# Kernel optimization log

Measured on AMD Instinct MI355X. Metric: run time of the kernel, lower is better.

The kernel has to match this reference:

```python
import jax, jax.numpy as jnp
import numpy as np

N, T, K, V, E = 64, 256, 64, 32000, 100


def setup_inputs() -> dict:
    key = jax.random.key(0)
    ks = jax.random.split(key, 7)
    x = jax.random.randint(ks[0], (N, T), 0, V)
    emb_weight = jax.random.normal(ks[1], (V, E), dtype=jnp.float32)
    # trans: Linear(E, K*K, bias=False), weight uniform(-1,1)
    W_trans = jax.random.uniform(ks[2], (K * K, E), minval=-1.0, maxval=1.0, dtype=jnp.float32)
    # start: Linear(1, K)
    start_w = jax.random.normal(ks[3], (K, 1), dtype=jnp.float32) * 0.1
    start_b = jax.random.normal(ks[4], (K,), dtype=jnp.float32) * 0.1
    # emb_cluster: Embedding(K, K)
    emb_cluster_w = jax.random.normal(ks[5], (K, K), dtype=jnp.float32)
    # vocab: Linear(K, V, bias=False), weight uniform(-1,1)
    vocab_w = jax.random.uniform(ks[6], (V, K), minval=-1.0, maxval=1.0, dtype=jnp.float32)
    return {"x": x, "emb_weight": emb_weight, "W_trans": W_trans,
            "start_w": start_w, "start_b": start_b,
            "emb_cluster_w": emb_cluster_w, "vocab_w": vocab_w}


def reference(x, emb_weight, W_trans, start_w, start_b, emb_cluster_w, vocab_w):
    n, t = x.shape
    k = emb_cluster_w.shape[0]
    # word embeddings used to condition transitions at steps 0..T-2
    xe = emb_weight[x[:, :-1]]                                   # [N,T-1,E]
    # transition log-probs: log_softmax over destination state
    tran = jax.nn.log_softmax(
        jnp.einsum('nte,ce->ntc', xe, W_trans).reshape(n, t - 1, k, k), axis=-1)
    # emission log-probs per cluster: E[k, v]
    Elog = jax.nn.log_softmax(emb_cluster_w @ vocab_w.T, axis=-1)  # [K,V]
    emit = Elog.T[x[:, 1:]]                                       # [N,T-1,K]
    # initial alpha: log_softmax(start(ones)) expanded over batch
    alpha0 = jax.nn.log_softmax(start_w[:, 0] + start_b)           # [K]
    alpha0 = jnp.broadcast_to(alpha0[None, :], (n, k))
    tran_t = jnp.moveaxis(tran, 1, 0)   # [T-1,N,K,K]
    emit_t = jnp.moveaxis(emit, 1, 0)   # [T-1,N,K]

    def step(alpha, te):
        tr, em = te
        # logsumexp over previous state j: alpha[n,j] + tr[n,j,k]
        a = jax.scipy.special.logsumexp(alpha[:, :, None] + tr, axis=1) + em
        return a, None

    alpha, _ = jax.lax.scan(step, alpha0, (tran_t, emit_t))
    return -jnp.mean(jax.scipy.special.logsumexp(alpha, axis=1))
```

## Files before the change

kernel.cpp:

```cpp
#include <hip/hip_runtime.h>
#include <hip/hip_bf16.h>
#include <stdint.h>

#define NT 16320
#define NTPAD 16384
#define KDIM 128
#define NCOLS 4096
#define NSEQ 64
#define TSTEPS 255
#define VOCAB 32000
#define EDIM 100
#define CHUNKS 17
#define CLEN 15

typedef __attribute__((ext_vector_type(8))) short s8v;
typedef __attribute__((ext_vector_type(4))) float f4v;

__device__ __forceinline__ float bflo(uint32_t u) { return __uint_as_float(u << 16); }
__device__ __forceinline__ float bfhi(uint32_t u) { return __uint_as_float(u & 0xffff0000u); }

__device__ __forceinline__ void load_lds16(const void* g, void* l) {
    __builtin_amdgcn_global_load_lds(
        (const __attribute__((address_space(1))) void*)(uintptr_t)g,
        (__attribute__((address_space(3))) void*)(uintptr_t)l,
        16, 0, 0);
}

__global__ __launch_bounds__(256) void prep_dk(const int* __restrict__ x,
                                               const float* __restrict__ emb,
                                               const float* __restrict__ Wt,
                                               const float* __restrict__ ec,
                                               const float* __restrict__ vw,
                                               __hip_bfloat16* __restrict__ A,
                                               __hip_bfloat16* __restrict__ B,
                                               float* __restrict__ partials) {
    int bid = blockIdx.x;
    int tid = threadIdx.x;
    if (bid < 1280) {
        int rloc = tid >> 4, q = tid & 15;
        int b = bid * 16 + rloc;
        int c0 = q * 8;
        float vals[8] = {0.f, 0.f, 0.f, 0.f, 0.f, 0.f, 0.f, 0.f};
        __hip_bfloat16* dst;
        if (b < NTPAD) {
            if (b < NT) {
                int n = b / TSTEPS;
                int t = b - n * TSTEPS;
                int tok = x[n * 256 + t];
                const float* er = emb + (size_t)tok * EDIM;
#pragma unroll
                for (int i = 0; i < 8; ++i) { int e = c0 + i; if (e < EDIM) vals[i] = er[e]; }
            }
            dst = A + (size_t)b * KDIM + c0;
        } else {
            int cc = b - NTPAD;
            const float* wr = Wt + (size_t)cc * EDIM;
#pragma unroll
            for (int i = 0; i < 8; ++i) { int e = c0 + i; if (e < EDIM) vals[i] = wr[e]; }
            dst = B + (size_t)cc * KDIM + c0;
        }
        union { __hip_bfloat16 h[8]; uint4 u; } pk;
#pragma unroll
        for (int i = 0; i < 8; ++i) pk.h[i] = __float2bfloat16(vals[i]);
        *(uint4*)dst = pk.u;
    } else {
        int db = bid - 1280;
        int wave = tid >> 6, lane = tid & 63;
        float er[64];
        {
            const float4* ecv = (const float4*)(ec + (size_t)lane * 64);
#pragma unroll
            for (int i = 0; i < 16; ++i) {
                float4 v = ecv[i];
                er[4 * i] = v.x; er[4 * i + 1] = v.y; er[4 * i + 2] = v.z; er[4 * i + 3] = v.w;
            }
        }
        int v0 = db * 125;
        float m = -1e30f, s = 0.f;
        for (int v = v0 + wave; v < v0 + 125; v += 4) {
            int vu = __builtin_amdgcn_readfirstlane(v);
            const float* row = vw + (size_t)vu * 64;
            float acc = 0.f;
#pragma unroll
            for (int e = 0; e < 64; ++e) acc += er[e] * row[e];
            float nm = fmaxf(m, acc);
            s = s * __expf(m - nm) + __expf(acc - nm);
            m = nm;
        }
        __shared__ float pm[4][64], ps[4][64];
        pm[wave][lane] = m; ps[wave][lane] = s;
        __syncthreads();
        if (tid < 64) {
            float M = pm[0][tid], Ssum = ps[0][tid];
#pragma unroll
            for (int w = 1; w < 4; ++w) {
                float m2 = pm[w][tid], s2 = ps[w][tid];
                float nm = fmaxf(M, m2);
                Ssum = Ssum * __expf(M - nm) + s2 * __expf(m2 - nm);
                M = nm;
            }
            partials[(db * 64 + tid) * 2]     = M;
            partials[(db * 64 + tid) * 2 + 1] = Ssum;
        }
    }
}

__global__ __launch_bounds__(256) void emit_kern(const int* __restrict__ x,
                                                 const float* __restrict__ ec,
                                                 const float* __restrict__ vw,
                                                 const float* __restrict__ partials,
                                                 __hip_bfloat16* __restrict__ emB) {
    __shared__ float pm[4][64], ps[4][64], sD[64];
    int tid = threadIdx.x;
    int wave = tid >> 6, lane = tid & 63;

    {
        float M = -1e30f, S = 0.f;
        for (int b = wave; b < 256; b += 4) {
            float m2 = partials[(b * 64 + lane) * 2];
            float s2 = partials[(b * 64 + lane) * 2 + 1];
            float nm = fmaxf(M, m2);
            S = S * __expf(M - nm) + s2 * __expf(m2 - nm);
            M = nm;
        }
        pm[wave][lane] = M; ps[wave][lane] = S;
    }

    float er[64];
    {
        const float4* ecv = (const float4*)(ec + (size_t)lane * 64);
#pragma unroll
        for (int i = 0; i < 16; ++i) {
            float4 v = ecv[i];
            er[4 * i] = v.x; er[4 * i + 1] = v.y; er[4 * i + 2] = v.z; er[4 * i + 3] = v.w;
        }
    }
    __syncthreads();
    if (tid < 64) {
        float M = pm[0][tid], S = ps[0][tid];
#pragma unroll
        for (int w = 1; w < 4; ++w) {
            float m2 = pm[w][tid], s2 = ps[w][tid];
            float nm = fmaxf(M, m2);
            S = S * __expf(M - nm) + s2 * __expf(m2 - nm);
            M = nm;
        }
        sD[tid] = M + __logf(S);
    }
    __syncthreads();

    float dj = sD[lane];
    int j = lane;
    int pos = ((j >> 2) & 3) * 16 + ((j >> 4) & 3) * 4 + (j & 3);
    int nt0 = blockIdx.x * 32 + wave * 8;
#pragma unroll
    for (int s = 0; s < 8; ++s) {
        int nt = nt0 + s;
        int n = nt / TSTEPS;
        int t = nt - n * TSTEPS;
        int tok = x[n * 256 + t + 1];
        tok = __builtin_amdgcn_readfirstlane(tok);
        const float* row = vw + (size_t)tok * 64;
        float acc = 0.f;
#pragma unroll
        for (int e = 0; e < 64; ++e) acc += er[e] * row[e];
        emB[(size_t)nt * 64 + pos] = __float2bfloat16(__expf(acc - dj));
    }
}

__global__ __launch_bounds__(256) void gemm_kern(const __hip_bfloat16* __restrict__ A,
                                                 const __hip_bfloat16* __restrict__ B,
                                                 const __hip_bfloat16* __restrict__ emB,
                                                 __hip_bfloat16* __restrict__ Eg) {
    int mblk = blockIdx.x;
    int nblk = blockIdx.y;
    int tid = threadIdx.x, wave = tid >> 6, lane = tid & 63;

    __shared__ __align__(16) char smem[65536];
    char* sA = smem;
    char* sB = smem + 32768;

    {
        int r0 = wave * 32;
        int l16 = lane & 15;
        int rsub = lane >> 4;
#pragma unroll
        for (int g = 0; g < 8; ++g) {
            int r = r0 + g * 4 + rsub;
            int chunk = l16 ^ (r & 7);
            const char* gp = (const char*)(A + (size_t)(mblk * 128 + r) * KDIM) + chunk * 16;
            load_lds16(gp, sA + (r0 + g * 4) * 256);
        }
#pragma unroll
        for (int g = 0; g < 8; ++g) {
            int c = r0 + g * 4 + rsub;
            int chunk = l16 ^ (c & 7);
            const char* gp = (const char*)(B + (size_t)(nblk * 128 + c) * KDIM) + chunk * 16;
            load_lds16(gp, sB + (r0 + g * 4) * 256);
        }
    }
    __syncthreads();

    int wc = (wave >> 1) * 64, wm = (wave & 1) * 64;
    int l15 = lane & 15, g4 = lane >> 4;
    f4v acc[4][4] = {};
#pragma unroll
    for (int k32 = 0; k32 < 4; ++k32) {
        s8v af[4], bf[4];
#pragma unroll
        for (int jt = 0; jt < 4; ++jt) {
            int r = wc + jt * 16 + l15;
            int chunk = (k32 * 4 + g4) ^ (r & 7);
            af[jt] = *(const s8v*)(sB + r * 256 + chunk * 16);
        }
#pragma unroll
        for (int mt = 0; mt < 4; ++mt) {
            int r = wm + mt * 16 + l15;
            int chunk = (k32 * 4 + g4) ^ (r & 7);
            bf[mt] = *(const s8v*)(sA + r * 256 + chunk * 16);
        }
#pragma unroll
        for (int jt = 0; jt < 4; ++jt)
#pragma unroll
            for (int mt = 0; mt < 4; ++mt)
                acc[jt][mt] = __builtin_amdgcn_mfma_f32_16x16x32_bf16(af[jt], bf[mt], acc[jt][mt], 0, 0, 0);
    }
    __syncthreads();

    char* sW = smem;
    const char* emb8 = (const char*)emB;
#pragma unroll
    for (int mt = 0; mt < 4; ++mt) {
        int mrow = wm + mt * 16 + l15;
        int mglob = mblk * 128 + mrow;
        float v[16];
#pragma unroll
        for (int jt = 0; jt < 4; ++jt)
#pragma unroll
            for (int rr = 0; rr < 4; ++rr) v[jt * 4 + rr] = acc[jt][mt][rr];
        float mx = v[0];
#pragma unroll
        for (int k = 1; k < 16; ++k) mx = fmaxf(mx, v[k]);
        mx = fmaxf(mx, __shfl_xor(mx, 16, 64));
        mx = fmaxf(mx, __shfl_xor(mx, 32, 64));
        float ex[16], sg = 0.f;
#pragma unroll
        for (int k = 0; k < 16; ++k) { ex[k] = __expf(v[k] - mx); sg += ex[k]; }
        sg += __shfl_xor(sg, 16, 64);
        sg += __shfl_xor(sg, 32, 64);
        float inv = 1.0f / sg;
        uint4 e0 = *(const uint4*)(emb8 + (size_t)mglob * 128 + g4 * 32);
        uint4 e1 = *(const uint4*)(emb8 + (size_t)mglob * 128 + g4 * 32 + 16);
        float em[16];
        {
            const uint32_t* w0 = (const uint32_t*)&e0;
            const uint32_t* w1 = (const uint32_t*)&e1;
#pragma unroll
            for (int i = 0; i < 4; ++i) {
                em[2 * i] = bflo(w0[i]);     em[2 * i + 1] = bfhi(w0[i]);
                em[8 + 2 * i] = bflo(w1[i]); em[8 + 2 * i + 1] = bfhi(w1[i]);
            }
        }
#pragma unroll
        for (int jt = 0; jt < 4; ++jt) {
            union { __hip_bfloat16 h[4]; uint2 u; } pk;
#pragma unroll
            for (int rr = 0; rr < 4; ++rr)
                pk.h[rr] = __float2bfloat16(ex[jt * 4 + rr] * inv * em[jt * 4 + rr]);
            *(uint2*)(sW + mrow * 272 + (wc + jt * 16 + g4 * 4) * 2) = pk.u;
        }
    }
    __syncthreads();

    {
        int rloc = tid >> 3;
        int q = tid & 7;
#pragma unroll
        for (int rp = 0; rp < 4; ++rp) {
            int row = rp * 32 + rloc;
            char* dst = (char*)Eg + (size_t)(mblk * 128 + row) * 8192 + nblk * 256;
            const char* src = sW + row * 272;
            *(uint4*)(dst + q * 16)       = *(const uint4*)(src + q * 16);
            *(uint4*)(dst + 128 + q * 16) = *(const uint4*)(src + 128 + q * 16);
        }
    }
}

__global__ __launch_bounds__(64) void chunk_kern(const __hip_bfloat16* __restrict__ Eg,
                                                 __hip_bfloat16* __restrict__ Gout,
                                                 float* __restrict__ Rout,
                                                 float* __restrict__ out) {
    int lane = threadIdx.x;
    if (blockIdx.x == 0 && lane == 0) *out = 0.f;
    int l15 = lane & 15, g4 = lane >> 4;
    int id = blockIdx.x;
    int n = (id * 3856) >> 16;
    int c = id - n * 17;
    int base_m = n * TSTEPS + c * CLEN;

    __shared__ __align__(16) char sGT[64 * 144];

    {
        uint4 z = {0, 0, 0, 0};
#pragma unroll
        for (int i = 0; i < 8; ++i) *(uint4*)(sGT + lane * 144 + i * 16) = z;
        *(uint16_t*)(sGT + lane * 144 + lane * 2) = 0x3F80;
    }

    const char* Ebase = (const char*)Eg;
    uint4 pf[4][2];
    {
        const char* tp = Ebase + (size_t)(base_m + 14) * 8192;
#pragma unroll
        for (int at = 0; at < 4; ++at)
#pragma unroll
            for (int kk = 0; kk < 2; ++kk)
                pf[at][kk] = *(const uint4*)(tp + (at * 16 + l15) * 128 + kk * 64 + g4 * 16);
    }

    float rlog[4] = {0.f, 0.f, 0.f, 0.f};

    for (int tl = 14; tl >= 0; --tl) {
        uint4 af[4][2];
#pragma unroll
        for (int at = 0; at < 4; ++at) { af[at][0] = pf[at][0]; af[at][1] = pf[at][1]; }
        if (tl > 0) {
            const char* tp = Ebase + (size_t)(base_m + tl - 1) * 8192;
#pragma unroll
            for (int at = 0; at < 4; ++at)
#pragma unroll
                for (int kk = 0; kk < 2; ++kk)
                    pf[at][kk] = *(const uint4*)(tp + (at * 16 + l15) * 128 + kk * 64 + g4 * 16);
        }

        f4v acc[4][4] = {};
#pragma unroll
        for (int kk = 0; kk < 2; ++kk) {
#pragma unroll
            for (int ct = 0; ct < 4; ++ct) {
                s8v b = *(const s8v*)(sGT + (ct * 16 + l15) * 144 + kk * 64 + g4 * 16);
#pragma unroll
                for (int at = 0; at < 4; ++at)
                    acc[at][ct] = __builtin_amdgcn_mfma_f32_16x16x32_bf16(
                        *(const s8v*)&af[at][kk], b, acc[at][ct], 0, 0, 0);
            }
        }

        if (tl % 3 == 0) {
#pragma unroll
            for (int ct = 0; ct < 4; ++ct) {
                float mx = acc[0][ct][0];
#pragma unroll
                for (int at = 0; at < 4; ++at)
#pragma unroll
                    for (int rr = 0; rr < 4; ++rr) mx = fmaxf(mx, acc[at][ct][rr]);
                mx = fmaxf(mx, __shfl_xor(mx, 16, 64));
                mx = fmaxf(mx, __shfl_xor(mx, 32, 64));
                mx = fmaxf(mx, 1e-38f);
                rlog[ct] += __logf(mx);
                float inv = 1.0f / mx;
                int col = ct * 16 + l15;
#pragma unroll
                for (int at = 0; at < 4; ++at) {
                    union { __hip_bfloat16 h[4]; uint2 u; } pk;
#pragma unroll
                    for (int rr = 0; rr < 4; ++rr)
                        pk.h[rr] = __float2bfloat16(acc[at][ct][rr] * inv);
                    *(uint2*)(sGT + col * 144 + at * 32 + g4 * 8) = pk.u;
                }
            }
        } else {
#pragma unroll
            for (int ct = 0; ct < 4; ++ct) {
                int col = ct * 16 + l15;
#pragma unroll
                for (int at = 0; at < 4; ++at) {
                    union { __hip_bfloat16 h[4]; uint2 u; } pk;
#pragma unroll
                    for (int rr = 0; rr < 4; ++rr)
                        pk.h[rr] = __float2bfloat16(acc[at][ct][rr]);
                    *(uint2*)(sGT + col * 144 + at * 32 + g4 * 8) = pk.u;
                }
            }
        }
    }

    {
        char* go = (char*)(Gout + (size_t)id * 4096 + lane * 64);
#pragma unroll
        for (int i = 0; i < 8; ++i)
            *(uint4*)(go + i * 16) = *(const uint4*)(sGT + lane * 144 + i * 16);
    }
    if (g4 == 0)
#pragma unroll
        for (int ct = 0; ct < 4; ++ct)
            Rout[(size_t)id * 64 + ct * 16 + l15] = rlog[ct];
}

__global__ __launch_bounds__(64) void combine_kern(const __hip_bfloat16* __restrict__ G,
                                                   const float* __restrict__ R,
                                                   const float* __restrict__ sw,
                                                   const float* __restrict__ sb,
                                                   float* __restrict__ out) {
    int n = blockIdx.x;
    int lane = threadIdx.x;
    __shared__ __align__(16) float sV[64];

    float alpha;
    {
        float v = sw[lane] + sb[lane];
        float m = v;
#pragma unroll
        for (int off = 1; off < 64; off <<= 1) m = fmaxf(m, __shfl_xor(m, off, 64));
        float s = __expf(v - m);
#pragma unroll
        for (int off = 1; off < 64; off <<= 1) s += __shfl_xor(s, off, 64);
        alpha = v - (m + __logf(s));
    }

    const char* Gb = (const char*)(G + (size_t)n * CHUNKS * 4096) + lane * 128;
    const float* Rb = R + (size_t)n * CHUNKS * 64 + lane;

    uint4 pf[8];
#pragma unroll
    for (int i = 0; i < 8; ++i) pf[i] = *(const uint4*)(Gb + i * 16);
    float rpf = Rb[0];

    for (int c = 0; c < CHUNKS; ++c) {
        uint4 cur[8];
#pragma unroll
        for (int i = 0; i < 8; ++i) cur[i] = pf[i];
        float rc = rpf;
        if (c + 1 < CHUNKS) {
            const char* gn = Gb + (size_t)(c + 1) * 8192;
#pragma unroll
            for (int i = 0; i < 8; ++i) pf[i] = *(const uint4*)(gn + i * 16);
            rpf = Rb[(c + 1) * 64];
        }

        float m = alpha;
#pragma unroll
        for (int off = 1; off < 64; off <<= 1) m = fmaxf(m, __shfl_xor(m, off, 64));
        sV[lane] = __expf(alpha - m);
        float acc = 0.f;
        const float4* sv4 = (const float4*)sV;
#pragma unroll
        for (int i = 0; i < 8; ++i) {
            const uint32_t* gw = (const uint32_t*)&cur[i];
            float4 va = sv4[2 * i], vb = sv4[2 * i + 1];
            acc += va.x * bflo(gw[0]) + va.y * bfhi(gw[0]);
            acc += va.z * bflo(gw[1]) + va.w * bfhi(gw[1]);
            acc += vb.x * bflo(gw[2]) + vb.y * bfhi(gw[2]);
            acc += vb.z * bflo(gw[3]) + vb.w * bfhi(gw[3]);
        }
        alpha = m + __logf(fmaxf(acc, 1e-38f)) + rc;
    }

    {
        float m = alpha;
#pragma unroll
        for (int off = 1; off < 64; off <<= 1) m = fmaxf(m, __shfl_xor(m, off, 64));
        float s = __expf(alpha - m);
#pragma unroll
        for (int off = 1; off < 64; off <<= 1) s += __shfl_xor(s, off, 64);
        if (lane == 0) atomicAdd(out, -(m + __logf(s)) * (1.0f / 64.0f));
    }
}

extern "C" void kernel_launch(void* const* d_in, const int* in_sizes, int n_in,
                              void* d_out, int out_size, void* d_ws, size_t ws_size,
                              hipStream_t stream) {
    const int*   x   = (const int*)d_in[0];
    const float* emb = (const float*)d_in[1];
    const float* Wt  = (const float*)d_in[2];
    const float* sw  = (const float*)d_in[3];
    const float* sb  = (const float*)d_in[4];
    const float* ec  = (const float*)d_in[5];
    const float* vw  = (const float*)d_in[6];
    float* out = (float*)d_out;
    char* ws = (char*)d_ws;

    __hip_bfloat16* Eg  = (__hip_bfloat16*)ws;
    __hip_bfloat16* A   = (__hip_bfloat16*)(ws + 134217728ull);
    __hip_bfloat16* B   = (__hip_bfloat16*)(ws + 138412032ull);
    __hip_bfloat16* emB = (__hip_bfloat16*)(ws + 139460608ull);
    float* partials     = (float*)(ws + 141557760ull);
    __hip_bfloat16* Gc  = (__hip_bfloat16*)(ws + 141688832ull);
    float* Rc           = (float*)(ws + 150601728ull);

    prep_dk<<<1536, 256, 0, stream>>>(x, emb, Wt, ec, vw, A, B, partials);
    emit_kern<<<510, 256, 0, stream>>>(x, ec, vw, partials, emB);
    gemm_kern<<<dim3(NTPAD / 128, NCOLS / 128), 256, 0, stream>>>(A, B, emB, Eg);
    chunk_kern<<<NSEQ * CHUNKS, 64, 0, stream>>>(Eg, Gc, Rc, out);
    combine_kern<<<NSEQ, 64, 0, stream>>>(Gc, Rc, sw, sb, out);
}
```

Measured before the change: 212.6 us.

## Fuse transition GEMM into chunked scan kernel, keep transition matrices in LDS

Merges the transition-matrix GEMM and the chunked scan into one kernel. Each block computes the 15 timestep transition matrices for its chunk straight into a swizzled LDS buffer, so the 128MB Eg intermediate no longer round-trips through global memory. The scan now runs across 4 waves, one column tile each, using about 129KB of dynamic LDS. In exchange, each block re-reads all of B from global/L2, and occupancy drops to one block per CU.

```diff
diff --git a/kernel.cpp b/kernel.cpp
--- a/kernel.cpp
+++ b/kernel.cpp
@@ -5,7 +5,6 @@
 #define NT 16320
 #define NTPAD 16384
 #define KDIM 128
-#define NCOLS 4096
 #define NSEQ 64
 #define TSTEPS 255
 #define VOCAB 32000
@@ -18,13 +17,6 @@
 
 __device__ __forceinline__ float bflo(uint32_t u) { return __uint_as_float(u << 16); }
 __device__ __forceinline__ float bfhi(uint32_t u) { return __uint_as_float(u & 0xffff0000u); }
-
-__device__ __forceinline__ void load_lds16(const void* g, void* l) {
-    __builtin_amdgcn_global_load_lds(
-        (const __attribute__((address_space(1))) void*)(uintptr_t)g,
-        (__attribute__((address_space(3))) void*)(uintptr_t)l,
-        16, 0, 0);
-}
 
 __global__ __launch_bounds__(256) void prep_dk(const int* __restrict__ x,
                                                const float* __restrict__ emb,
@@ -168,76 +160,74 @@
     }
 }
 
-__global__ __launch_bounds__(256) void gemm_kern(const __hip_bfloat16* __restrict__ A,
-                                                 const __hip_bfloat16* __restrict__ B,
-                                                 const __hip_bfloat16* __restrict__ emB,
-                                                 __hip_bfloat16* __restrict__ Eg) {
-    int mblk = blockIdx.x;
-    int nblk = blockIdx.y;
-    int tid = threadIdx.x, wave = tid >> 6, lane = tid & 63;
-
-    __shared__ __align__(16) char smem[65536];
-    char* sA = smem;
-    char* sB = smem + 32768;
-
-    {
-        int r0 = wave * 32;
-        int l16 = lane & 15;
-        int rsub = lane >> 4;
-#pragma unroll
-        for (int g = 0; g < 8; ++g) {
-            int r = r0 + g * 4 + rsub;
-            int chunk = l16 ^ (r & 7);
-            const char* gp = (const char*)(A + (size_t)(mblk * 128 + r) * KDIM) + chunk * 16;
-            load_lds16(gp, sA + (r0 + g * 4) * 256);
-        }
-#pragma unroll
-        for (int g = 0; g < 8; ++g) {
-            int c = r0 + g * 4 + rsub;
-            int chunk = l16 ^ (c & 7);
-            const char* gp = (const char*)(B + (size_t)(nblk * 128 + c) * KDIM) + chunk * 16;
-            load_lds16(gp, sB + (r0 + g * 4) * 256);
-        }
-    }
-    __syncthreads();
-
-    int wc = (wave >> 1) * 64, wm = (wave & 1) * 64;
+__global__ __launch_bounds__(256, 1) void fused_kern(const __hip_bfloat16* __restrict__ A,
+                                                     const __hip_bfloat16* __restrict__ B,
+                                                     const __hip_bfloat16* __restrict__ emB,
+                                                     __hip_bfloat16* __restrict__ Gout,
+                                                     float* __restrict__ Rout,
+                                                     float* __restrict__ out) {
+    extern __shared__ __align__(16) char smem[];
+    char* sE  = smem;
+    char* sGT = smem + 122880;
+
+    int tid = threadIdx.x;
+    int wave = tid >> 6, lane = tid & 63;
     int l15 = lane & 15, g4 = lane >> 4;
-    f4v acc[4][4] = {};
-#pragma unroll
-    for (int k32 = 0; k32 < 4; ++k32) {
-        s8v af[4], bf[4];
-#pragma unroll
-        for (int jt = 0; jt < 4; ++jt) {
-            int r = wc + jt * 16 + l15;
-            int chunk = (k32 * 4 + g4) ^ (r & 7);
-            af[jt] = *(const s8v*)(sB + r * 256 + chunk * 16);
-        }
-#pragma unroll
-        for (int mt = 0; mt < 4; ++mt) {
-            int r = wm + mt * 16 + l15;
-            int chunk = (k32 * 4 + g4) ^ (r & 7);
-            bf[mt] = *(const s8v*)(sA + r * 256 + chunk * 16);
-        }
+    int id = blockIdx.x;
+    if (id == 0 && tid == 0) *out = 0.f;
+    int n = (id * 3856) >> 16;
+    int c = id - n * 17;
+    int base_m = n * TSTEPS + c * CLEN;
+
+    if (wave == 0) {
+        uint4 z = {0, 0, 0, 0};
+#pragma unroll
+        for (int i = 0; i < 8; ++i) *(uint4*)(sGT + lane * 144 + i * 16) = z;
+        *(uint16_t*)(sGT + lane * 144 + lane * 2) = 0x3F80;
+    }
+
+    const char* Ac = (const char*)A;
+    s8v bfx[4];
+#pragma unroll
+    for (int k32 = 0; k32 < 4; ++k32)
+        bfx[k32] = *(const s8v*)(Ac + (size_t)(base_m + l15) * 256 + k32 * 64 + g4 * 16);
+
+    float em[16];
+    {
+        const char* ep = (const char*)emB + (size_t)(base_m + l15) * 128 + g4 * 32;
+        uint4 e0 = *(const uint4*)ep;
+        uint4 e1 = *(const uint4*)(ep + 16);
+        const uint32_t* w0 = (const uint32_t*)&e0;
+        const uint32_t* w1 = (const uint32_t*)&e1;
+#pragma unroll
+        for (int i = 0; i < 4; ++i) {
+            em[2 * i] = bflo(w0[i]);     em[2 * i + 1] = bfhi(w0[i]);
+            em[8 + 2 * i] = bflo(w1[i]); em[8 + 2 * i + 1] = bfhi(w1[i]);
+        }
+    }
+
+    const char* Bc = (const char*)B;
+    for (int grp = 0; grp < 16; ++grp) {
+        int gidx = wave * 16 + grp;
+        int cbase = gidx * 64;
+        s8v af[4][4];
 #pragma unroll
         for (int jt = 0; jt < 4; ++jt)
 #pragma unroll
-            for (int mt = 0; mt < 4; ++mt)
-                acc[jt][mt] = __builtin_amdgcn_mfma_f32_16x16x32_bf16(af[jt], bf[mt], acc[jt][mt], 0, 0, 0);
-    }
-    __syncthreads();
-
-    char* sW = smem;
-    const char* emb8 = (const char*)emB;
-#pragma unroll
-    for (int mt = 0; mt < 4; ++mt) {
-        int mrow = wm + mt * 16 + l15;
-        int mglob = mblk * 128 + mrow;
+            for (int k32 = 0; k32 < 4; ++k32)
+                af[jt][k32] = *(const s8v*)(Bc + (size_t)(cbase + jt * 16 + l15) * 256 + k32 * 64 + g4 * 16);
+        f4v acc[4] = {};
+#pragma unroll
+        for (int k32 = 0; k32 < 4; ++k32)
+#pragma unroll
+            for (int jt = 0; jt < 4; ++jt)
+                acc[jt] = __builtin_amdgcn_mfma_f32_16x16x32_bf16(af[jt][k32], bfx[k32], acc[jt], 0, 0, 0);
+
         float v[16];
 #pragma unroll
         for (int jt = 0; jt < 4; ++jt)
 #pragma unroll
-            for (int rr = 0; rr < 4; ++rr) v[jt * 4 + rr] = acc[jt][mt][rr];
+            for (int rr = 0; rr < 4; ++rr) v[jt * 4 + rr] = acc[jt][rr];
         float mx = v[0];
 #pragma unroll
         for (int k = 1; k < 16; ++k) mx = fmaxf(mx, v[k]);
@@ -249,152 +239,83 @@
         sg += __shfl_xor(sg, 16, 64);
         sg += __shfl_xor(sg, 32, 64);
         float inv = 1.0f / sg;
-        uint4 e0 = *(const uint4*)(emb8 + (size_t)mglob * 128 + g4 * 32);
-        uint4 e1 = *(const uint4*)(emb8 + (size_t)mglob * 128 + g4 * 32 + 16);
-        float em[16];
-        {
-            const uint32_t* w0 = (const uint32_t*)&e0;
-            const uint32_t* w1 = (const uint32_t*)&e1;
-#pragma unroll
-            for (int i = 0; i < 4; ++i) {
-                em[2 * i] = bflo(w0[i]);     em[2 * i + 1] = bfhi(w0[i]);
-                em[8 + 2 * i] = bflo(w1[i]); em[8 + 2 * i + 1] = bfhi(w1[i]);
-            }
-        }
-#pragma unroll
-        for (int jt = 0; jt < 4; ++jt) {
-            union { __hip_bfloat16 h[4]; uint2 u; } pk;
-#pragma unroll
-            for (int rr = 0; rr < 4; ++rr)
-                pk.h[rr] = __float2bfloat16(ex[jt * 4 + rr] * inv * em[jt * 4 + rr]);
-            *(uint2*)(sW + mrow * 272 + (wc + jt * 16 + g4 * 4) * 2) = pk.u;
+        if (l15 < 15) {
+            int swz = ((l15 ^ gidx) & 7) << 4;
+#pragma unroll
+            for (int jt = 0; jt < 4; ++jt) {
+                union { __hip_bfloat16 h[4]; uint2 u; } pk;
+#pragma unroll
+                for (int rr = 0; rr < 4; ++rr)
+                    pk.h[rr] = __float2bfloat16(ex[jt * 4 + rr] * inv * em[jt * 4 + rr]);
+                int off = l15 * 8192 + (cbase + jt * 16 + g4 * 4) * 2;
+                *(uint2*)(sE + (off ^ swz)) = pk.u;
+            }
         }
     }
     __syncthreads();
 
-    {
-        int rloc = tid >> 3;
-        int q = tid & 7;
-#pragma unroll
-        for (int rp = 0; rp < 4; ++rp) {
-            int row = rp * 32 + rloc;
-            char* dst = (char*)Eg + (size_t)(mblk * 128 + row) * 8192 + nblk * 256;
-            const char* src = sW + row * 272;
-            *(uint4*)(dst + q * 16)       = *(const uint4*)(src + q * 16);
-            *(uint4*)(dst + 128 + q * 16) = *(const uint4*)(src + 128 + q * 16);
-        }
-    }
-}
-
-__global__ __launch_bounds__(64) void chunk_kern(const __hip_bfloat16* __restrict__ Eg,
-                                                 __hip_bfloat16* __restrict__ Gout,
-                                                 float* __restrict__ Rout,
-                                                 float* __restrict__ out) {
-    int lane = threadIdx.x;
-    if (blockIdx.x == 0 && lane == 0) *out = 0.f;
-    int l15 = lane & 15, g4 = lane >> 4;
-    int id = blockIdx.x;
-    int n = (id * 3856) >> 16;
-    int c = id - n * 17;
-    int base_m = n * TSTEPS + c * CLEN;
-
-    __shared__ __align__(16) char sGT[64 * 144];
-
-    {
-        uint4 z = {0, 0, 0, 0};
-#pragma unroll
-        for (int i = 0; i < 8; ++i) *(uint4*)(sGT + lane * 144 + i * 16) = z;
-        *(uint16_t*)(sGT + lane * 144 + lane * 2) = 0x3F80;
-    }
-
-    const char* Ebase = (const char*)Eg;
-    uint4 pf[4][2];
-    {
-        const char* tp = Ebase + (size_t)(base_m + 14) * 8192;
+    int ct = wave;
+    int colrow = (ct * 16 + l15) * 144;
+    float rlog = 0.f;
+    for (int tl = 14; tl >= 0; --tl) {
+        int swz = ((tl ^ l15) & 7) << 4;
+        s8v af[4][2];
 #pragma unroll
         for (int at = 0; at < 4; ++at)
 #pragma unroll
-            for (int kk = 0; kk < 2; ++kk)
-                pf[at][kk] = *(const uint4*)(tp + (at * 16 + l15) * 128 + kk * 64 + g4 * 16);
-    }
-
-    float rlog[4] = {0.f, 0.f, 0.f, 0.f};
-
-    for (int tl = 14; tl >= 0; --tl) {
-        uint4 af[4][2];
-#pragma unroll
-        for (int at = 0; at < 4; ++at) { af[at][0] = pf[at][0]; af[at][1] = pf[at][1]; }
-        if (tl > 0) {
-            const char* tp = Ebase + (size_t)(base_m + tl - 1) * 8192;
+            for (int kk = 0; kk < 2; ++kk) {
+                int off = tl * 8192 + (at * 16 + l15) * 128 + kk * 64 + g4 * 16;
+                af[at][kk] = *(const s8v*)(sE + (off ^ swz));
+            }
+        s8v bG[2];
+#pragma unroll
+        for (int kk = 0; kk < 2; ++kk)
+            bG[kk] = *(const s8v*)(sGT + colrow + kk * 64 + g4 * 16);
+        f4v acc[4] = {};
+#pragma unroll
+        for (int kk = 0; kk < 2; ++kk)
 #pragma unroll
             for (int at = 0; at < 4; ++at)
-#pragma unroll
-                for (int kk = 0; kk < 2; ++kk)
-                    pf[at][kk] = *(const uint4*)(tp + (at * 16 + l15) * 128 + kk * 64 + g4 * 16);
-        }
-
-        f4v acc[4][4] = {};
-#pragma unroll
-        for (int kk = 0; kk < 2; ++kk) {
-#pragma unroll
-            for (int ct = 0; ct < 4; ++ct) {
-                s8v b = *(const s8v*)(sGT + (ct * 16 + l15) * 144 + kk * 64 + g4 * 16);
-#pragma unroll
-                for (int at = 0; at < 4; ++at)
-                    acc[at][ct] = __builtin_amdgcn_mfma_f32_16x16x32_bf16(
-                        *(const s8v*)&af[at][kk], b, acc[at][ct], 0, 0, 0);
-            }
-        }
+                acc[at] = __builtin_amdgcn_mfma_f32_16x16x32_bf16(af[at][kk], bG[kk], acc[at], 0, 0, 0);
 
         if (tl % 3 == 0) {
-#pragma unroll
-            for (int ct = 0; ct < 4; ++ct) {
-                float mx = acc[0][ct][0];
-#pragma unroll
-                for (int at = 0; at < 4; ++at)
-#pragma unroll
-                    for (int rr = 0; rr < 4; ++rr) mx = fmaxf(mx, acc[at][ct][rr]);
-                mx = fmaxf(mx, __shfl_xor(mx, 16, 64));
-                mx = fmaxf(mx, __shfl_xor(mx, 32, 64));
-                mx = fmaxf(mx, 1e-38f);
-                rlog[ct] += __logf(mx);
-                float inv = 1.0f / mx;
-                int col = ct * 16 + l15;
-#pragma unroll
-                for (int at = 0; at < 4; ++at) {
-                    union { __hip_bfloat16 h[4]; uint2 u; } pk;
-#pragma unroll
-                    for (int rr = 0; rr < 4; ++rr)
-                        pk.h[rr] = __float2bfloat16(acc[at][ct][rr] * inv);
-                    *(uint2*)(sGT + col * 144 + at * 32 + g4 * 8) = pk.u;
-                }
+            float mx = acc[0][0];
+#pragma unroll
+            for (int at = 0; at < 4; ++at)
+#pragma unroll
+                for (int rr = 0; rr < 4; ++rr) mx = fmaxf(mx, acc[at][rr]);
+            mx = fmaxf(mx, __shfl_xor(mx, 16, 64));
+            mx = fmaxf(mx, __shfl_xor(mx, 32, 64));
+            mx = fmaxf(mx, 1e-38f);
+            rlog += __logf(mx);
+            float inv = 1.0f / mx;
+#pragma unroll
+            for (int at = 0; at < 4; ++at) {
+                union { __hip_bfloat16 h[4]; uint2 u; } pk;
+#pragma unroll
+                for (int rr = 0; rr < 4; ++rr)
+                    pk.h[rr] = __float2bfloat16(acc[at][rr] * inv);
+                *(uint2*)(sGT + colrow + at * 32 + g4 * 8) = pk.u;
             }
         } else {
 #pragma unroll
-            for (int ct = 0; ct < 4; ++ct) {
-                int col = ct * 16 + l15;
-#pragma unroll
-                for (int at = 0; at < 4; ++at) {
-                    union { __hip_bfloat16 h[4]; uint2 u; } pk;
-#pragma unroll
-                    for (int rr = 0; rr < 4; ++rr)
-                        pk.h[rr] = __float2bfloat16(acc[at][ct][rr]);
-                    *(uint2*)(sGT + col * 144 + at * 32 + g4 * 8) = pk.u;
-                }
-            }
-        }
-    }
-
-    {
-        char* go = (char*)(Gout + (size_t)id * 4096 + lane * 64);
-#pragma unroll
-        for (int i = 0; i < 8; ++i)
-            *(uint4*)(go + i * 16) = *(const uint4*)(sGT + lane * 144 + i * 16);
-    }
-    if (g4 == 0)
-#pragma unroll
-        for (int ct = 0; ct < 4; ++ct)
-            Rout[(size_t)id * 64 + ct * 16 + l15] = rlog[ct];
+            for (int at = 0; at < 4; ++at) {
+                union { __hip_bfloat16 h[4]; uint2 u; } pk;
+#pragma unroll
+                for (int rr = 0; rr < 4; ++rr)
+                    pk.h[rr] = __float2bfloat16(acc[at][rr]);
+                *(uint2*)(sGT + colrow + at * 32 + g4 * 8) = pk.u;
+            }
+        }
+    }
+
+    {
+        char* go = (char*)(Gout + (size_t)id * 4096) + (ct * 16 + l15) * 128 + g4 * 32;
+        const char* src = sGT + colrow + g4 * 32;
+        *(uint4*)go        = *(const uint4*)src;
+        *(uint4*)(go + 16) = *(const uint4*)(src + 16);
+    }
+    if (g4 == 0) Rout[(size_t)id * 64 + ct * 16 + l15] = rlog;
 }
 
 __global__ __launch_bounds__(64) void combine_kern(const __hip_bfloat16* __restrict__ G,
@@ -480,17 +401,22 @@
     float* out = (float*)d_out;
     char* ws = (char*)d_ws;
 
-    __hip_bfloat16* Eg  = (__hip_bfloat16*)ws;
-    __hip_bfloat16* A   = (__hip_bfloat16*)(ws + 134217728ull);
-    __hip_bfloat16* B   = (__hip_bfloat16*)(ws + 138412032ull);
-    __hip_bfloat16* emB = (__hip_bfloat16*)(ws + 139460608ull);
-    float* partials     = (float*)(ws + 141557760ull);
-    __hip_bfloat16* Gc  = (__hip_bfloat16*)(ws + 141688832ull);
-    float* Rc           = (float*)(ws + 150601728ull);
+    __hip_bfloat16* A   = (__hip_bfloat16*)ws;
+    __hip_bfloat16* B   = (__hip_bfloat16*)(ws + 4194304ull);
+    __hip_bfloat16* emB = (__hip_bfloat16*)(ws + 5242880ull);
+    float* partials     = (float*)(ws + 7340032ull);
+    __hip_bfloat16* Gc  = (__hip_bfloat16*)(ws + 7471104ull);
+    float* Rc           = (float*)(ws + 16384000ull);
+
+    static int ldsInit = 0;
+    if (!ldsInit) {
+        hipFuncSetAttribute((const void*)fused_kern,
+                            hipFuncAttributeMaxDynamicSharedMemorySize, 132096);
+        ldsInit = 1;
+    }
 
     prep_dk<<<1536, 256, 0, stream>>>(x, emb, Wt, ec, vw, A, B, partials);
     emit_kern<<<510, 256, 0, stream>>>(x, ec, vw, partials, emB);
-    gemm_kern<<<dim3(NTPAD / 128, NCOLS / 128), 256, 0, stream>>>(A, B, emB, Eg);
-    chunk_kern<<<NSEQ * CHUNKS, 64, 0, stream>>>(Eg, Gc, Rc, out);
+    fused_kern<<<NSEQ * CHUNKS, 256, 132096, stream>>>(A, B, emB, Gc, Rc, out);
     combine_kern<<<NSEQ, 64, 0, stream>>>(Gc, Rc, sw, sb, out);
 }
```

New measurement: 317.9 us. +49.5%, slower.

## Merge emission and GEMM kernels, fold combine into chunk kernel via counters

Applied to the files above, without the earlier changes.

The emission kernel now runs as extra blocks inside the transition GEMM launch, so the GEMM no longer needs emission probabilities. The emission scaling moves into the chunk kernel, which applies it when it builds chunk products. The separate combine kernel is replaced by a last-block-done atomic counter, so the chunk kernel itself finishes the alpha recursion. The vocab normaliser drops its max subtraction and uses a plain exp sum. Together these remove two kernel launches and the dependency bubbles between them, at the cost of overflow risk in the unshifted exp and extra emB reads in the chunk stage.

```diff
diff --git a/kernel.cpp b/kernel.cpp
--- a/kernel.cpp
+++ b/kernel.cpp
@@ -5,7 +5,6 @@
 #define NT 16320
 #define NTPAD 16384
 #define KDIM 128
-#define NCOLS 4096
 #define NSEQ 64
 #define TSTEPS 255
 #define VOCAB 32000
@@ -33,7 +32,9 @@
                                                const float* __restrict__ vw,
                                                __hip_bfloat16* __restrict__ A,
                                                __hip_bfloat16* __restrict__ B,
-                                               float* __restrict__ partials) {
+                                               float* __restrict__ partials,
+                                               int* __restrict__ cnt,
+                                               float* __restrict__ out) {
     int bid = blockIdx.x;
     int tid = threadIdx.x;
     if (bid < 1280) {
@@ -66,6 +67,10 @@
     } else {
         int db = bid - 1280;
         int wave = tid >> 6, lane = tid & 63;
+        if (db == 0 && tid < 64) {
+            cnt[tid] = 0;
+            if (tid == 0) *out = 0.f;
+        }
         float er[64];
         {
             const float4* ecv = (const float4*)(ec + (size_t)lane * 64);
@@ -76,222 +81,176 @@
             }
         }
         int v0 = db * 125;
-        float m = -1e30f, s = 0.f;
+        float S = 0.f;
         for (int v = v0 + wave; v < v0 + 125; v += 4) {
             int vu = __builtin_amdgcn_readfirstlane(v);
             const float* row = vw + (size_t)vu * 64;
             float acc = 0.f;
 #pragma unroll
             for (int e = 0; e < 64; ++e) acc += er[e] * row[e];
-            float nm = fmaxf(m, acc);
-            s = s * __expf(m - nm) + __expf(acc - nm);
-            m = nm;
-        }
-        __shared__ float pm[4][64], ps[4][64];
-        pm[wave][lane] = m; ps[wave][lane] = s;
-        __syncthreads();
-        if (tid < 64) {
-            float M = pm[0][tid], Ssum = ps[0][tid];
-#pragma unroll
-            for (int w = 1; w < 4; ++w) {
-                float m2 = pm[w][tid], s2 = ps[w][tid];
-                float nm = fmaxf(M, m2);
-                Ssum = Ssum * __expf(M - nm) + s2 * __expf(m2 - nm);
-                M = nm;
-            }
-            partials[(db * 64 + tid) * 2]     = M;
-            partials[(db * 64 + tid) * 2 + 1] = Ssum;
-        }
+            S += __expf(acc);
+        }
+        __shared__ float ps[4][64];
+        ps[wave][lane] = S;
+        __syncthreads();
+        if (tid < 64)
+            partials[db * 64 + tid] = ps[0][tid] + ps[1][tid] + ps[2][tid] + ps[3][tid];
     }
 }
 
-__global__ __launch_bounds__(256) void emit_kern(const int* __restrict__ x,
+__global__ __launch_bounds__(256) void gemm_emit(const __hip_bfloat16* __restrict__ A,
+                                                 const __hip_bfloat16* __restrict__ B,
+                                                 const int* __restrict__ x,
                                                  const float* __restrict__ ec,
                                                  const float* __restrict__ vw,
                                                  const float* __restrict__ partials,
+                                                 __hip_bfloat16* __restrict__ Eg,
                                                  __hip_bfloat16* __restrict__ emB) {
-    __shared__ float pm[4][64], ps[4][64], sD[64];
-    int tid = threadIdx.x;
-    int wave = tid >> 6, lane = tid & 63;
-
-    {
-        float M = -1e30f, S = 0.f;
-        for (int b = wave; b < 256; b += 4) {
-            float m2 = partials[(b * 64 + lane) * 2];
-            float s2 = partials[(b * 64 + lane) * 2 + 1];
-            float nm = fmaxf(M, m2);
-            S = S * __expf(M - nm) + s2 * __expf(m2 - nm);
-            M = nm;
-        }
-        pm[wave][lane] = M; ps[wave][lane] = S;
-    }
-
-    float er[64];
-    {
-        const float4* ecv = (const float4*)(ec + (size_t)lane * 64);
-#pragma unroll
-        for (int i = 0; i < 16; ++i) {
-            float4 v = ecv[i];
-            er[4 * i] = v.x; er[4 * i + 1] = v.y; er[4 * i + 2] = v.z; er[4 * i + 3] = v.w;
-        }
-    }
-    __syncthreads();
-    if (tid < 64) {
-        float M = pm[0][tid], S = ps[0][tid];
-#pragma unroll
-        for (int w = 1; w < 4; ++w) {
-            float m2 = pm[w][tid], s2 = ps[w][tid];
-            float nm = fmaxf(M, m2);
-            S = S * __expf(M - nm) + s2 * __expf(m2 - nm);
-            M = nm;
-        }
-        sD[tid] = M + __logf(S);
-    }
-    __syncthreads();
-
-    float dj = sD[lane];
-    int j = lane;
-    int pos = ((j >> 2) & 3) * 16 + ((j >> 4) & 3) * 4 + (j & 3);
-    int nt0 = blockIdx.x * 32 + wave * 8;
-#pragma unroll
-    for (int s = 0; s < 8; ++s) {
-        int nt = nt0 + s;
-        int n = nt / TSTEPS;
-        int t = nt - n * TSTEPS;
-        int tok = x[n * 256 + t + 1];
-        tok = __builtin_amdgcn_readfirstlane(tok);
-        const float* row = vw + (size_t)tok * 64;
-        float acc = 0.f;
-#pragma unroll
-        for (int e = 0; e < 64; ++e) acc += er[e] * row[e];
-        emB[(size_t)nt * 64 + pos] = __float2bfloat16(__expf(acc - dj));
+    __shared__ __align__(16) char smem[65536];
+    int bid = blockIdx.x;
+    int tid = threadIdx.x, wave = tid >> 6, lane = tid & 63;
+
+    if (bid < 4096) {
+        int mblk = bid & 127;
+        int nblk = bid >> 7;
+        char* sA = smem;
+        char* sB = smem + 32768;
+
+        {
+            int r0 = wave * 32;
+            int l16 = lane & 15;
+            int rsub = lane >> 4;
+#pragma unroll
+            for (int g = 0; g < 8; ++g) {
+                int r = r0 + g * 4 + rsub;
+                int chunk = l16 ^ (r & 7);
+                const char* gp = (const char*)(A + (size_t)(mblk * 128 + r) * KDIM) + chunk * 16;
+                load_lds16(gp, sA + (r0 + g * 4) * 256);
+            }
+#pragma unroll
+            for (int g = 0; g < 8; ++g) {
+                int c = r0 + g * 4 + rsub;
+                int chunk = l16 ^ (c & 7);
+                const char* gp = (const char*)(B + (size_t)(nblk * 128 + c) * KDIM) + chunk * 16;
+                load_lds16(gp, sB + (r0 + g * 4) * 256);
+            }
+        }
+        __syncthreads();
+
+        int wc = (wave >> 1) * 64, wm = (wave & 1) * 64;
+        int l15 = lane & 15, g4 = lane >> 4;
+        f4v acc[4][4] = {};
+#pragma unroll
+        for (int k32 = 0; k32 < 4; ++k32) {
+            s8v af[4], bf[4];
+#pragma unroll
+            for (int jt = 0; jt < 4; ++jt) {
+                int r = wc + jt * 16 + l15;
+                int chunk = (k32 * 4 + g4) ^ (r & 7);
+                af[jt] = *(const s8v*)(sB + r * 256 + chunk * 16);
+            }
+#pragma unroll
+            for (int mt = 0; mt < 4; ++mt) {
+                int r = wm + mt * 16 + l15;
+                int chunk = (k32 * 4 + g4) ^ (r & 7);
+                bf[mt] = *(const s8v*)(sA + r * 256 + chunk * 16);
+            }
+#pragma unroll
+            for (int jt = 0; jt < 4; ++jt)
+#pragma unroll
+                for (int mt = 0; mt < 4; ++mt)
+                    acc[jt][mt] = __builtin_amdgcn_mfma_f32_16x16x32_bf16(af[jt], bf[mt], acc[jt][mt], 0, 0, 0);
+        }
+        __syncthreads();
+
+        char* sW = smem;
+#pragma unroll
+        for (int mt = 0; mt < 4; ++mt) {
+            int mrow = wm + mt * 16 + l15;
+            float v[16];
+#pragma unroll
+            for (int jt = 0; jt < 4; ++jt)
+#pragma unroll
+                for (int rr = 0; rr < 4; ++rr) v[jt * 4 + rr] = acc[jt][mt][rr];
+            float mx = v[0];
+#pragma unroll
+            for (int k = 1; k < 16; ++k) mx = fmaxf(mx, v[k]);
+            mx = fmaxf(mx, __shfl_xor(mx, 16, 64));
+            mx = fmaxf(mx, __shfl_xor(mx, 32, 64));
+            float ex[16], sg = 0.f;
+#pragma unroll
+            for (int k = 0; k < 16; ++k) { ex[k] = __expf(v[k] - mx); sg += ex[k]; }
+            sg += __shfl_xor(sg, 16, 64);
+            sg += __shfl_xor(sg, 32, 64);
+            float inv = 1.0f / sg;
+#pragma unroll
+            for (int jt = 0; jt < 4; ++jt) {
+                union { __hip_bfloat16 h[4]; uint2 u; } pk;
+#pragma unroll
+                for (int rr = 0; rr < 4; ++rr)
+                    pk.h[rr] = __float2bfloat16(ex[jt * 4 + rr] * inv);
+                *(uint2*)(sW + mrow * 272 + (wc + jt * 16 + g4 * 4) * 2) = pk.u;
+            }
+        }
+        __syncthreads();
+
+        {
+            int rloc = tid >> 3;
+            int q = tid & 7;
+#pragma unroll
+            for (int rp = 0; rp < 4; ++rp) {
+                int row = rp * 32 + rloc;
+                char* dst = (char*)Eg + (size_t)(mblk * 128 + row) * 8192 + nblk * 256;
+                const char* src = sW + row * 272;
+                *(uint4*)(dst + q * 16)       = *(const uint4*)(src + q * 16);
+                *(uint4*)(dst + 128 + q * 16) = *(const uint4*)(src + 128 + q * 16);
+            }
+        }
+    } else {
+        int bid2 = bid - 4096;
+        float* sEC = (float*)smem;
+        float* sP  = (float*)(smem + 16640);
+        float* sD  = (float*)(smem + 17664);
+        for (int i = tid; i < 4096; i += 256) {
+            int r = i >> 6, cc = i & 63;
+            sEC[r * 65 + cc] = ec[i];
+        }
+        float S = 0.f;
+        for (int b = wave * 64; b < wave * 64 + 64; ++b) S += partials[b * 64 + lane];
+        sP[wave * 64 + lane] = S;
+        __syncthreads();
+        if (tid < 64) sD[tid] = __logf(sP[tid] + sP[64 + tid] + sP[128 + tid] + sP[192 + tid]);
+        __syncthreads();
+
+        float dj = sD[lane];
+        int j = lane;
+        int pos = ((j >> 2) & 3) * 16 + ((j >> 4) & 3) * 4 + (j & 3);
+        int nt0 = bid2 * 32 + wave * 8;
+#pragma unroll
+        for (int s = 0; s < 8; ++s) {
+            int nt = nt0 + s;
+            int n = nt / TSTEPS;
+            int t = nt - n * TSTEPS;
+            int tok = x[n * 256 + t + 1];
+            tok = __builtin_amdgcn_readfirstlane(tok);
+            const float* row = vw + (size_t)tok * 64;
+            float acc = 0.f;
+#pragma unroll
+            for (int e = 0; e < 64; ++e) acc += sEC[lane * 65 + e] * row[e];
+            emB[(size_t)nt * 64 + pos] = __float2bfloat16(__expf(acc - dj));
+        }
     }
 }
 
-__global__ __launch_bounds__(256) void gemm_kern(const __hip_bfloat16* __restrict__ A,
-                                                 const __hip_bfloat16* __restrict__ B,
+__global__ __launch_bounds__(64) void chunk_comb(const __hip_bfloat16* __restrict__ Eg,
                                                  const __hip_bfloat16* __restrict__ emB,
-                                                 __hip_bfloat16* __restrict__ Eg) {
-    int mblk = blockIdx.x;
-    int nblk = blockIdx.y;
-    int tid = threadIdx.x, wave = tid >> 6, lane = tid & 63;
-
-    __shared__ __align__(16) char smem[65536];
-    char* sA = smem;
-    char* sB = smem + 32768;
-
-    {
-        int r0 = wave * 32;
-        int l16 = lane & 15;
-        int rsub = lane >> 4;
-#pragma unroll
-        for (int g = 0; g < 8; ++g) {
-            int r = r0 + g * 4 + rsub;
-            int chunk = l16 ^ (r & 7);
-            const char* gp = (const char*)(A + (size_t)(mblk * 128 + r) * KDIM) + chunk * 16;
-            load_lds16(gp, sA + (r0 + g * 4) * 256);
-        }
-#pragma unroll
-        for (int g = 0; g < 8; ++g) {
-            int c = r0 + g * 4 + rsub;
-            int chunk = l16 ^ (c & 7);
-            const char* gp = (const char*)(B + (size_t)(nblk * 128 + c) * KDIM) + chunk * 16;
-            load_lds16(gp, sB + (r0 + g * 4) * 256);
-        }
-    }
-    __syncthreads();
-
-    int wc = (wave >> 1) * 64, wm = (wave & 1) * 64;
-    int l15 = lane & 15, g4 = lane >> 4;
-    f4v acc[4][4] = {};
-#pragma unroll
-    for (int k32 = 0; k32 < 4; ++k32) {
-        s8v af[4], bf[4];
-#pragma unroll
-        for (int jt = 0; jt < 4; ++jt) {
-            int r = wc + jt * 16 + l15;
-            int chunk = (k32 * 4 + g4) ^ (r & 7);
-            af[jt] = *(const s8v*)(sB + r * 256 + chunk * 16);
-        }
-#pragma unroll
-        for (int mt = 0; mt < 4; ++mt) {
-            int r = wm + mt * 16 + l15;
-            int chunk = (k32 * 4 + g4) ^ (r & 7);
-            bf[mt] = *(const s8v*)(sA + r * 256 + chunk * 16);
-        }
-#pragma unroll
-        for (int jt = 0; jt < 4; ++jt)
-#pragma unroll
-            for (int mt = 0; mt < 4; ++mt)
-                acc[jt][mt] = __builtin_amdgcn_mfma_f32_16x16x32_bf16(af[jt], bf[mt], acc[jt][mt], 0, 0, 0);
-    }
-    __syncthreads();
-
-    char* sW = smem;
-    const char* emb8 = (const char*)emB;
-#pragma unroll
-    for (int mt = 0; mt < 4; ++mt) {
-        int mrow = wm + mt * 16 + l15;
-        int mglob = mblk * 128 + mrow;
-        float v[16];
-#pragma unroll
-        for (int jt = 0; jt < 4; ++jt)
-#pragma unroll
-            for (int rr = 0; rr < 4; ++rr) v[jt * 4 + rr] = acc[jt][mt][rr];
-        float mx = v[0];
-#pragma unroll
-        for (int k = 1; k < 16; ++k) mx = fmaxf(mx, v[k]);
-        mx = fmaxf(mx, __shfl_xor(mx, 16, 64));
-        mx = fmaxf(mx, __shfl_xor(mx, 32, 64));
-        float ex[16], sg = 0.f;
-#pragma unroll
-        for (int k = 0; k < 16; ++k) { ex[k] = __expf(v[k] - mx); sg += ex[k]; }
-        sg += __shfl_xor(sg, 16, 64);
-        sg += __shfl_xor(sg, 32, 64);
-        float inv = 1.0f / sg;
-        uint4 e0 = *(const uint4*)(emb8 + (size_t)mglob * 128 + g4 * 32);
-        uint4 e1 = *(const uint4*)(emb8 + (size_t)mglob * 128 + g4 * 32 + 16);
-        float em[16];
-        {
-            const uint32_t* w0 = (const uint32_t*)&e0;
-            const uint32_t* w1 = (const uint32_t*)&e1;
-#pragma unroll
-            for (int i = 0; i < 4; ++i) {
-                em[2 * i] = bflo(w0[i]);     em[2 * i + 1] = bfhi(w0[i]);
-                em[8 + 2 * i] = bflo(w1[i]); em[8 + 2 * i + 1] = bfhi(w1[i]);
-            }
-        }
-#pragma unroll
-        for (int jt = 0; jt < 4; ++jt) {
-            union { __hip_bfloat16 h[4]; uint2 u; } pk;
-#pragma unroll
-            for (int rr = 0; rr < 4; ++rr)
-                pk.h[rr] = __float2bfloat16(ex[jt * 4 + rr] * inv * em[jt * 4 + rr]);
-            *(uint2*)(sW + mrow * 272 + (wc + jt * 16 + g4 * 4) * 2) = pk.u;
-        }
-    }
-    __syncthreads();
-
-    {
-        int rloc = tid >> 3;
-        int q = tid & 7;
-#pragma unroll
-        for (int rp = 0; rp < 4; ++rp) {
-            int row = rp * 32 + rloc;
-            char* dst = (char*)Eg + (size_t)(mblk * 128 + row) * 8192 + nblk * 256;
-            const char* src = sW + row * 272;
-            *(uint4*)(dst + q * 16)       = *(const uint4*)(src + q * 16);
-            *(uint4*)(dst + 128 + q * 16) = *(const uint4*)(src + 128 + q * 16);
-        }
-    }
-}
-
-__global__ __launch_bounds__(64) void chunk_kern(const __hip_bfloat16* __restrict__ Eg,
-                                                 __hip_bfloat16* __restrict__ Gout,
-                                                 float* __restrict__ Rout,
-                                                 float* __restrict__ out) {
+                                                 __hip_bfloat16* Gout,
+                                                 float* Rout,
+                                                 const float* __restrict__ sw,
+                                                 const float* __restrict__ sb,
+                                                 int* cnt,
+                                                 float* out) {
     int lane = threadIdx.x;
-    if (blockIdx.x == 0 && lane == 0) *out = 0.f;
     int l15 = lane & 15, g4 = lane >> 4;
     int id = blockIdx.x;
     int n = (id * 3856) >> 16;
@@ -304,7 +263,9 @@
         uint4 z = {0, 0, 0, 0};
 #pragma unroll
         for (int i = 0; i < 8; ++i) *(uint4*)(sGT + lane * 144 + i * 16) = z;
-        *(uint16_t*)(sGT + lane * 144 + lane * 2) = 0x3F80;
+        int pos_l = ((lane >> 2) & 3) * 16 + ((lane >> 4) & 3) * 4 + (lane & 3);
+        *(uint16_t*)(sGT + lane * 144 + lane * 2) =
+            *(const uint16_t*)((const char*)emB + (size_t)(base_m + 14) * 128 + pos_l * 2);
     }
 
     const char* Ebase = (const char*)Eg;
@@ -333,6 +294,14 @@
                     pf[at][kk] = *(const uint4*)(tp + (at * 16 + l15) * 128 + kk * 64 + g4 * 16);
         }
 
+        uint4 e0, e1;
+        {
+            int trow = base_m + (tl > 0 ? tl - 1 : 0);
+            const char* ep = (const char*)emB + (size_t)trow * 128 + g4 * 32;
+            e0 = *(const uint4*)ep;
+            e1 = *(const uint4*)(ep + 16);
+        }
+
         f4v acc[4][4] = {};
 #pragma unroll
         for (int kk = 0; kk < 2; ++kk) {
@@ -344,6 +313,21 @@
                     acc[at][ct] = __builtin_amdgcn_mfma_f32_16x16x32_bf16(
                         *(const s8v*)&af[at][kk], b, acc[at][ct], 0, 0, 0);
             }
+        }
+
+        float em[16];
+        {
+            const uint32_t* w0 = (const uint32_t*)&e0;
+            const uint32_t* w1 = (const uint32_t*)&e1;
+#pragma unroll
+            for (int i = 0; i < 4; ++i) {
+                em[2 * i] = bflo(w0[i]);     em[2 * i + 1] = bfhi(w0[i]);
+                em[8 + 2 * i] = bflo(w1[i]); em[8 + 2 * i + 1] = bfhi(w1[i]);
+            }
+        }
+        if (tl == 0) {
+#pragma unroll
+            for (int k = 0; k < 16; ++k) em[k] = 1.0f;
         }
 
         if (tl % 3 == 0) {
@@ -365,7 +349,7 @@
                     union { __hip_bfloat16 h[4]; uint2 u; } pk;
 #pragma unroll
                     for (int rr = 0; rr < 4; ++rr)
-                        pk.h[rr] = __float2bfloat16(acc[at][ct][rr] * inv);
+                        pk.h[rr] = __float2bfloat16(acc[at][ct][rr] * inv * em[at * 4 + rr]);
                     *(uint2*)(sGT + col * 144 + at * 32 + g4 * 8) = pk.u;
                 }
             }
@@ -378,7 +362,7 @@
                     union { __hip_bfloat16 h[4]; uint2 u; } pk;
 #pragma unroll
                     for (int rr = 0; rr < 4; ++rr)
-                        pk.h[rr] = __float2bfloat16(acc[at][ct][rr]);
+                        pk.h[rr] = __float2bfloat16(acc[at][ct][rr] * em[at * 4 + rr]);
                     *(uint2*)(sGT + col * 144 + at * 32 + g4 * 8) = pk.u;
                 }
             }
@@ -395,16 +379,15 @@
 #pragma unroll
         for (int ct = 0; ct < 4; ++ct)
             Rout[(size_t)id * 64 + ct * 16 + l15] = rlog[ct];
-}
-
-__global__ __launch_bounds__(64) void combine_kern(const __hip_bfloat16* __restrict__ G,
-                                                   const float* __restrict__ R,
-                                                   const float* __restrict__ sw,
-                                                   const float* __restrict__ sb,
-                                                   float* __restrict__ out) {
-    int n = blockIdx.x;
-    int lane = threadIdx.x;
-    __shared__ __align__(16) float sV[64];
+
+    __threadfence();
+    int old = 0;
+    if (lane == 0) old = atomicAdd(&cnt[n], 1);
+    old = __shfl(old, 0, 64);
+    if (old != CHUNKS - 1) return;
+    __threadfence();
+
+    float* sV = (float*)sGT;
 
     float alpha;
     {
@@ -418,42 +401,42 @@
         alpha = v - (m + __logf(s));
     }
 
-    const char* Gb = (const char*)(G + (size_t)n * CHUNKS * 4096) + lane * 128;
-    const float* Rb = R + (size_t)n * CHUNKS * 64 + lane;
-
-    uint4 pf[8];
-#pragma unroll
-    for (int i = 0; i < 8; ++i) pf[i] = *(const uint4*)(Gb + i * 16);
+    const char* Gb = (const char*)(Gout + (size_t)n * CHUNKS * 4096) + lane * 128;
+    const float* Rb = Rout + (size_t)n * CHUNKS * 64 + lane;
+
+    uint4 pfc[8];
+#pragma unroll
+    for (int i = 0; i < 8; ++i) pfc[i] = *(const uint4*)(Gb + i * 16);
     float rpf = Rb[0];
 
-    for (int c = 0; c < CHUNKS; ++c) {
+    for (int cc = 0; cc < CHUNKS; ++cc) {
         uint4 cur[8];
 #pragma unroll
-        for (int i = 0; i < 8; ++i) cur[i] = pf[i];
+        for (int i = 0; i < 8; ++i) cur[i] = pfc[i];
         float rc = rpf;
-        if (c + 1 < CHUNKS) {
-            const char* gn = Gb + (size_t)(c + 1) * 8192;
-#pragma unroll
-            for (int i = 0; i < 8; ++i) pf[i] = *(const uint4*)(gn + i * 16);
-            rpf = Rb[(c + 1) * 64];
+        if (cc + 1 < CHUNKS) {
+            const char* gn = Gb + (size_t)(cc + 1) * 8192;
+#pragma unroll
+            for (int i = 0; i < 8; ++i) pfc[i] = *(const uint4*)(gn + i * 16);
+            rpf = Rb[(cc + 1) * 64];
         }
 
         float m = alpha;
 #pragma unroll
         for (int off = 1; off < 64; off <<= 1) m = fmaxf(m, __shfl_xor(m, off, 64));
         sV[lane] = __expf(alpha - m);
-        float acc = 0.f;
+        float acc2 = 0.f;
         const float4* sv4 = (const float4*)sV;
 #pragma unroll
         for (int i = 0; i < 8; ++i) {
             const uint32_t* gw = (const uint32_t*)&cur[i];
             float4 va = sv4[2 * i], vb = sv4[2 * i + 1];
-            acc += va.x * bflo(gw[0]) + va.y * bfhi(gw[0]);
-            acc += va.z * bflo(gw[1]) + va.w * bfhi(gw[1]);
-            acc += vb.x * bflo(gw[2]) + vb.y * bfhi(gw[2]);
-            acc += vb.z * bflo(gw[3]) + vb.w * bfhi(gw[3]);
-        }
-        alpha = m + __logf(fmaxf(acc, 1e-38f)) + rc;
+            acc2 += va.x * bflo(gw[0]) + va.y * bfhi(gw[0]);
+            acc2 += va.z * bflo(gw[1]) + va.w * bfhi(gw[1]);
+            acc2 += vb.x * bflo(gw[2]) + vb.y * bfhi(gw[2]);
+            acc2 += vb.z * bflo(gw[3]) + vb.w * bfhi(gw[3]);
+        }
+        alpha = m + __logf(fmaxf(acc2, 1e-38f)) + rc;
     }
 
     {
@@ -485,12 +468,11 @@
     __hip_bfloat16* B   = (__hip_bfloat16*)(ws + 138412032ull);
     __hip_bfloat16* emB = (__hip_bfloat16*)(ws + 139460608ull);
     float* partials     = (float*)(ws + 141557760ull);
-    __hip_bfloat16* Gc  = (__hip_bfloat16*)(ws + 141688832ull);
-    float* Rc           = (float*)(ws + 150601728ull);
-
-    prep_dk<<<1536, 256, 0, stream>>>(x, emb, Wt, ec, vw, A, B, partials);
-    emit_kern<<<510, 256, 0, stream>>>(x, ec, vw, partials, emB);
-    gemm_kern<<<dim3(NTPAD / 128, NCOLS / 128), 256, 0, stream>>>(A, B, emB, Eg);
-    chunk_kern<<<NSEQ * CHUNKS, 64, 0, stream>>>(Eg, Gc, Rc, out);
-    combine_kern<<<NSEQ, 64, 0, stream>>>(Gc, Rc, sw, sb, out);
+    __hip_bfloat16* Gc  = (__hip_bfloat16*)(ws + 141623296ull);
+    float* Rc           = (float*)(ws + 150536192ull);
+    int*   cnt          = (int*)(ws + 150814720ull);
+
+    prep_dk<<<1536, 256, 0, stream>>>(x, emb, Wt, ec, vw, A, B, partials, cnt, out);
+    gemm_emit<<<4606, 256, 0, stream>>>(A, B, x, ec, vw, partials, Eg, emB);
+    chunk_comb<<<1088, 64, 0, stream>>>(Eg, emB, Gc, Rc, sw, sb, cnt, out);
 }
```

New measurement: 316.9 us. 49.0% more time.
